# Performance work log

Measured on AMD Instinct MI355X. Metric: run time of the kernel, lower is better.

Reference implementation:

```python
import jax, jax.numpy as jnp
import numpy as np

N = 6144       # nodes
E = 12288      # edges (~2N for a sparse simplicial complex)
NF = 32        # node features
EF = 16        # edge features
NH = [32, 32]  # node_hidden
EH = [16, 16]  # edge_hidden
EPS = 1e-5


def setup_inputs() -> dict:
    key = jax.random.key(0)
    ks = jax.random.split(key, 24)
    s = 0.1  # weight init scale
    inp = {}
    inp["X_n"] = jax.random.normal(ks[0], (N, NF), jnp.float32)
    inp["X_e"] = jax.random.normal(ks[1], (E, EF), jnp.float32)
    # normalized adjacency-like operator (non-negative, row mass ~1)
    inp["A_tilde"] = jax.random.uniform(ks[2], (N, N), jnp.float32) * (1.0 / N)
    # normalized Hodge-1 Laplacian-like operator
    inp["L1_tilde"] = jax.random.normal(ks[3], (E, E), jnp.float32) * (1.0 / np.sqrt(E))
    # incidence-like operator
    inp["B1"] = jax.random.normal(ks[4], (N, E), jnp.float32) * (1.0 / np.sqrt(E))
    # GNN linear layers: weight [out, in] (torch convention)
    inp["gnn_W0"] = jax.random.normal(ks[5], (NH[0], NF), jnp.float32) * s
    inp["gnn_b0"] = jnp.zeros((NH[0],), jnp.float32)
    inp["gnn_W1"] = jax.random.normal(ks[6], (NH[1], NH[0]), jnp.float32) * s
    inp["gnn_b1"] = jnp.zeros((NH[1],), jnp.float32)
    # HoSC layer 0: theta in=EF out=EH[0], BN params
    inp["th_W0"] = jax.random.normal(ks[7], (EH[0], EF), jnp.float32) * s
    inp["th_b0"] = jnp.zeros((EH[0],), jnp.float32)
    inp["bn_g0"] = jnp.ones((EH[0],), jnp.float32)
    inp["bn_b0"] = jnp.zeros((EH[0],), jnp.float32)
    # HoSC layer 1: input collapses to 1 channel (max keepdim)
    inp["th_W1"] = jax.random.normal(ks[8], (EH[1], 1), jnp.float32) * s
    inp["th_b1"] = jnp.zeros((EH[1],), jnp.float32)
    inp["bn_g1"] = jnp.ones((EH[1],), jnp.float32)
    inp["bn_b1"] = jnp.zeros((EH[1],), jnp.float32)
    # head: fc1 in = NH[-1] + len(EH) = 34, out = 2N; fc2 out = 1
    inp["fc1_W"] = jax.random.normal(ks[9], (2 * N, NH[-1] + len(EH)), jnp.float32) * s
    inp["fc1_b"] = jnp.zeros((2 * N,), jnp.float32)
    inp["fc2_W"] = jax.random.normal(ks[10], (1, 2 * N), jnp.float32) * s
    inp["fc2_b"] = jnp.zeros((1,), jnp.float32)
    return inp


def _gnn_layer(A, H, W, b):
    # H <- relu((A @ H) @ W^T + b)
    return jax.nn.relu(jnp.matmul(jnp.matmul(A, H), W.T) + b)


def _hosc_layer(Z, L1, W, b, g, beta):
    Zt = jnp.matmul(Z, W.T) + b            # theta
    Zc = jnp.matmul(L1, Zt)                # Laplacian conv
    m = jnp.mean(Zc, axis=0)               # BatchNorm1d (training-mode batch stats)
    v = jnp.var(Zc, axis=0)
    Zp = jax.nn.relu(g * (Zc - m) * jax.lax.rsqrt(v + EPS) + beta)
    return jnp.max(Zp, axis=1, keepdims=True)  # [E, 1]


def reference(X_n, X_e, A_tilde, L1_tilde, B1,
              gnn_W0, gnn_b0, gnn_W1, gnn_b1,
              th_W0, th_b0, bn_g0, bn_b0,
              th_W1, th_b1, bn_g1, bn_b1,
              fc1_W, fc1_b, fc2_W, fc2_b):
    # GNN over nodes
    H = _gnn_layer(A_tilde, X_n, gnn_W0, gnn_b0)
    H_n = _gnn_layer(A_tilde, H, gnn_W1, gnn_b1)      # [N, NH[-1]]
    # HoSC over edges
    Z0 = _hosc_layer(X_e, L1_tilde, th_W0, th_b0, bn_g0, bn_b0)  # [E, 1]
    Z1 = _hosc_layer(Z0, L1_tilde, th_W1, th_b1, bn_g1, bn_b1)   # [E, 1]
    Z_cat = jnp.concatenate([Z0, Z1], axis=1)         # [E, 2]
    H_e = jnp.matmul(B1, Z_cat)                       # [N, 2]
    # head
    Hcat = jnp.concatenate([H_n, H_e], axis=1)        # [N, 34]
    f = jax.nn.relu(jnp.matmul(Hcat, fc1_W.T) + fc1_b)
    f = jnp.matmul(f, fc2_W.T) + fc2_b                # [N, 1]
    return jax.nn.sigmoid(f).squeeze(-1)              # [N]
```

## Files before the change

kernel.cpp:

```cpp
#include <hip/hip_runtime.h>
#include <hip/hip_cooperative_groups.h>
#include <math.h>

namespace cg = cooperative_groups;

#define NND 6144
#define NED 12288
#define GRID 1024
static constexpr float EPS_BN = 1e-5f;

#define HN_OFF    0
#define HE_OFF    196608
#define ST_OFF    208896
#define Y_OFF     208960
#define T0_OFF    405568
#define ZT_OFF    602176
#define ZC_OFF    798784
#define Z0_OFF    995392
#define Z1_OFF    1007680
#define U_OFF     1019968
#define S_OFF     1032256
#define PP_OFF    1044544

typedef float floatx4 __attribute__((ext_vector_type(4)));

__device__ __forceinline__ float4 ntload4(const float* p) {
  floatx4 v = __builtin_nontemporal_load(reinterpret_cast<const floatx4*>(p));
  return make_float4(v.x, v.y, v.z, v.w);
}
__device__ __forceinline__ float4 ld4(const float* p) {
  return *reinterpret_cast<const float4*>(p);
}
__device__ __forceinline__ void gll16(const float* g, float* l) {
  __builtin_amdgcn_global_load_lds(
      (const __attribute__((address_space(1))) unsigned int*)g,
      (__attribute__((address_space(3))) unsigned int*)l, 16, 0, 0);
}

struct Params {
  const float *X_n, *X_e, *A, *L1, *B1;
  const float *gW0, *gb0, *gW1, *gb1;
  const float *tW0, *tb0, *bng0, *bnb0;
  const float *tW1, *tb1, *bng1, *bnb1;
  const float *fc1W, *fc1b, *fc2W, *fc2b;
  float *ws;
  float *out;
};

template<int PHASE>
__global__ __launch_bounds__(256)
__attribute__((amdgpu_waves_per_eu(4, 4)))
void pipeline(Params p) {
  __shared__ float lds[10240];
  float* sst = &lds[10176];
  float* red = &lds[10208];

  const int tid  = threadIdx.x;
  const int lane = tid & 63;
  const int w    = tid >> 6;
  const int blk  = blockIdx.x;
  const int gtid = blk * 256 + tid;
  constexpr bool ALL = (PHASE == 0);

  float* Hn = p.ws + HN_OFF;
  float* he = p.ws + HE_OFF;
  float* st = p.ws + ST_OFF;
  float* Y  = p.ws + Y_OFF;
  float* T0 = p.ws + T0_OFF;
  float* ZT = p.ws + ZT_OFF;
  float* ZC = p.ws + ZC_OFF;
  float* Z0 = p.ws + Z0_OFF;
  float* Z1 = p.ws + Z1_OFF;
  float* u  = p.ws + U_OFF;
  float* s  = p.ws + S_OFF;
  float* pp = p.ws + PP_OFF;

  auto gemm32 = [&](const float* bias, float* outp) {
    const int rg = w >> 1, cg_ = w & 1;
    const int r0 = blk * 6;
    const int c0 = cg_ * 16;
    float acc[3][16];
    #pragma unroll
    for (int r = 0; r < 3; ++r)
      #pragma unroll
      for (int c = 0; c < 16; ++c) acc[r][c] = 0.f;

    for (int kb = 0; kb < NND; kb += 256) {
      #pragma unroll
      for (int i = 0; i < 8; ++i) {
        const int yr = w * 8 + i;
        gll16(Y + (size_t)yr * NND + kb + lane * 4, &lds[yr * 256]);
      }
      #pragma unroll
      for (int i = 0; i < 2; ++i) {
        const int ar = w * 2 + i;
        if (ar < 6)
          gll16(p.A + (size_t)(r0 + ar) * NND + kb + lane * 4, &lds[8192 + ar * 256]);
      }
      __syncthreads();
      float4 av[3];
      #pragma unroll
      for (int r = 0; r < 3; ++r)
        av[r] = ld4(&lds[8192 + (rg * 3 + r) * 256 + lane * 4]);
      #pragma unroll
      for (int c = 0; c < 16; ++c) {
        const float4 y = ld4(&lds[(c0 + c) * 256 + lane * 4]);
        #pragma unroll
        for (int r = 0; r < 3; ++r) {
          acc[r][c] = fmaf(av[r].x, y.x, acc[r][c]);
          acc[r][c] = fmaf(av[r].y, y.y, acc[r][c]);
          acc[r][c] = fmaf(av[r].z, y.z, acc[r][c]);
          acc[r][c] = fmaf(av[r].w, y.w, acc[r][c]);
        }
      }
      __syncthreads();
    }
    #pragma unroll
    for (int r = 0; r < 3; ++r) {
      float wv[16];
      #pragma unroll
      for (int c = 0; c < 16; ++c) {
        float t = acc[r][c] + __shfl_xor(acc[r][c], 32, 64);
        wv[c] = t + __shfl_xor(t, 16, 64);
      }
      #pragma unroll
      for (int b = 3; b >= 0; --b) {
        const int m = 1 << b;
        const bool hi = (lane & m) != 0;
        #pragma unroll
        for (int i = 0; i < (1 << b); ++i) {
          float x = wv[i], yv = wv[i + (1 << b)];
          float send = hi ? x : yv;
          float recv = __shfl_xor(send, m, 64);
          wv[i] = (hi ? yv : x) + recv;
        }
      }
      if (lane < 16) {
        float v = fmaxf(wv[0] + bias[c0 + lane], 0.f);
        outp[(size_t)(r0 + rg * 3 + r) * 32 + c0 + lane] = v;
      }
    }
  };

  if constexpr (ALL || PHASE == 1) {
    if (blk == 0 && tid < 64) st[tid] = 0.f;
    if (gtid < NND) {
      const int m = gtid;
      float x[32];
      #pragma unroll
      for (int k = 0; k < 32; k += 4) {
        float4 v = ld4(p.X_n + (size_t)m * 32 + k);
        x[k] = v.x; x[k+1] = v.y; x[k+2] = v.z; x[k+3] = v.w;
      }
      #pragma unroll
      for (int oc = 0; oc < 32; ++oc) {
        float acc = 0.f;
        #pragma unroll
        for (int k = 0; k < 32; ++k) acc = fmaf(x[k], p.gW0[oc * 32 + k], acc);
        Y[(size_t)oc * NND + m] = acc;
      }
    } else if (gtid < NND + NED) {
      const int e = gtid - NND;
      float x[16];
      #pragma unroll
      for (int k = 0; k < 16; k += 4) {
        float4 v = ld4(p.X_e + (size_t)e * 16 + k);
        x[k] = v.x; x[k+1] = v.y; x[k+2] = v.z; x[k+3] = v.w;
      }
      #pragma unroll
      for (int oc = 0; oc < 16; ++oc) {
        float acc = p.tb0[oc];
        #pragma unroll
        for (int k = 0; k < 16; ++k) acc = fmaf(x[k], p.tW0[oc * 16 + k], acc);
        ZT[(size_t)oc * NED + e] = acc;
      }
    }
  }
  if constexpr (ALL) cg::this_grid().sync();

  if constexpr (ALL || PHASE == 2) {
    gemm32(p.gb0, T0);

    const int r0 = blk * 12;
    float acc[3][16];
    #pragma unroll
    for (int r = 0; r < 3; ++r)
      #pragma unroll
      for (int c = 0; c < 16; ++c) acc[r][c] = 0.f;

    for (int kb = 0; kb < NED; kb += 256) {
      #pragma unroll
      for (int i = 0; i < 4; ++i) {
        const int yr = w * 4 + i;
        gll16(ZT + (size_t)yr * NED + kb + lane * 4, &lds[yr * 256]);
      }
      #pragma unroll
      for (int i = 0; i < 3; ++i) {
        const int ar = w * 3 + i;
        gll16(p.L1 + (size_t)(r0 + ar) * NED + kb + lane * 4, &lds[4096 + ar * 256]);
      }
      __syncthreads();
      float4 av[3];
      #pragma unroll
      for (int r = 0; r < 3; ++r)
        av[r] = ld4(&lds[4096 + (w * 3 + r) * 256 + lane * 4]);
      #pragma unroll
      for (int c = 0; c < 16; ++c) {
        const float4 y = ld4(&lds[c * 256 + lane * 4]);
        #pragma unroll
        for (int r = 0; r < 3; ++r) {
          acc[r][c] = fmaf(av[r].x, y.x, acc[r][c]);
          acc[r][c] = fmaf(av[r].y, y.y, acc[r][c]);
          acc[r][c] = fmaf(av[r].z, y.z, acc[r][c]);
          acc[r][c] = fmaf(av[r].w, y.w, acc[r][c]);
        }
      }
      __syncthreads();
    }
    float stS = 0.f, stQ = 0.f;
    #pragma unroll
    for (int r = 0; r < 3; ++r) {
      float wv[16];
      #pragma unroll
      for (int c = 0; c < 16; ++c) {
        float t = acc[r][c] + __shfl_xor(acc[r][c], 32, 64);
        wv[c] = t + __shfl_xor(t, 16, 64);
      }
      #pragma unroll
      for (int b = 3; b >= 0; --b) {
        const int m = 1 << b;
        const bool hi = (lane & m) != 0;
        #pragma unroll
        for (int i = 0; i < (1 << b); ++i) {
          float x = wv[i], yv = wv[i + (1 << b)];
          float send = hi ? x : yv;
          float recv = __shfl_xor(send, m, 64);
          wv[i] = (hi ? yv : x) + recv;
        }
      }
      if (lane < 16) {
        const float v = wv[0];
        ZC[(size_t)(r0 + w * 3 + r) * 16 + lane] = v;
        stS += v; stQ += v * v;
      }
    }
    if (tid < 32) sst[tid] = 0.f;
    __syncthreads();
    if (lane < 16) {
      atomicAdd(&sst[lane], stS);
      atomicAdd(&sst[16 + lane], stQ);
    }
    __syncthreads();
    if (tid < 32) atomicAdd(st + tid, sst[tid]);
  }
  if constexpr (ALL) cg::this_grid().sync();

  if constexpr (ALL || PHASE == 3) {
    if (gtid < NND) {
      const int m = gtid;
      float x[32];
      #pragma unroll
      for (int k = 0; k < 32; k += 4) {
        float4 v = ld4(T0 + (size_t)m * 32 + k);
        x[k] = v.x; x[k+1] = v.y; x[k+2] = v.z; x[k+3] = v.w;
      }
      #pragma unroll
      for (int oc = 0; oc < 32; ++oc) {
        float acc = 0.f;
        #pragma unroll
        for (int k = 0; k < 32; ++k) acc = fmaf(x[k], p.gW1[oc * 32 + k], acc);
        Y[(size_t)oc * NND + m] = acc;
      }
    } else if (gtid < NND + NED) {
      const int e = gtid - NND;
      const float invE = 1.f / (float)NED;
      float best = -3.4e38f;
      #pragma unroll
      for (int c = 0; c < 16; ++c) {
        float m = st[c] * invE;
        float var = st[16 + c] * invE - m * m;
        float sc = p.bng0[c] * rsqrtf(var + EPS_BN);
        float sh = p.bnb0[c] - m * sc;
        best = fmaxf(best, fmaf(ZC[(size_t)e * 16 + c], sc, sh));
      }
      Z0[e] = fmaxf(best, 0.f);
    }
  }
  if constexpr (ALL) cg::this_grid().sync();

  if constexpr (ALL || PHASE == 4) {
    gemm32(p.gb1, Hn);

    const int rb = GRID - 1 - blk;
    const int r0 = rb * 12 + w * 3;
    const float* mp[3];
    #pragma unroll
    for (int r = 0; r < 3; ++r) mp[r] = p.L1 + (size_t)(r0 + r) * NED;
    float ua[3] = {0,0,0}, sa[3] = {0,0,0};
    float4 a[3], an[3];
    #pragma unroll
    for (int r = 0; r < 3; ++r) a[r] = ntload4(mp[r] + lane * 4);
    float4 z = ld4(Z0 + lane * 4), zn;
    for (int kb = 0; kb < NED; kb += 256) {
      const int k = kb + lane * 4;
      const bool more = (kb + 256) < NED;
      if (more) {
        #pragma unroll
        for (int r = 0; r < 3; ++r) an[r] = ntload4(mp[r] + k + 256);
        zn = ld4(Z0 + k + 256);
      }
      #pragma unroll
      for (int r = 0; r < 3; ++r) {
        ua[r] += a[r].x*z.x + a[r].y*z.y + a[r].z*z.z + a[r].w*z.w;
        sa[r] += a[r].x + a[r].y + a[r].z + a[r].w;
      }
      if (more) {
        #pragma unroll
        for (int r = 0; r < 3; ++r) a[r] = an[r];
        z = zn;
      }
    }
    #pragma unroll
    for (int r = 0; r < 3; ++r)
      #pragma unroll
      for (int m = 1; m < 64; m <<= 1) {
        ua[r] += __shfl_xor(ua[r], m, 64);
        sa[r] += __shfl_xor(sa[r], m, 64);
      }
    if (lane == 0) {
      float s1 = 0.f, s2 = 0.f, s3 = 0.f, s4 = 0.f, s5 = 0.f;
      #pragma unroll
      for (int r = 0; r < 3; ++r) {
        u[r0 + r] = ua[r]; s[r0 + r] = sa[r];
        s1 += ua[r]; s2 += sa[r];
        s3 += ua[r] * ua[r]; s4 += sa[r] * sa[r]; s5 += ua[r] * sa[r];
      }
      red[w * 5 + 0] = s1; red[w * 5 + 1] = s2; red[w * 5 + 2] = s3;
      red[w * 5 + 3] = s4; red[w * 5 + 4] = s5;
    }
    __syncthreads();
    if (tid < 5)
      atomicAdd(st + 32 + tid, red[tid] + red[5 + tid] + red[10 + tid] + red[15 + tid]);
  }
  if constexpr (ALL) cg::this_grid().sync();

  if constexpr (ALL || PHASE == 5) {
    if (gtid < NED) {
      const int e = gtid;
      const float invE = 1.f / (float)NED;
      const float Su = st[32], Ss = st[33], Suu = st[34], Sss = st[35], Sus = st[36];
      const float uu = u[e], ssv = s[e];
      float best = -3.4e38f;
      #pragma unroll
      for (int c = 0; c < 16; ++c) {
        const float wc = p.tW1[c], bc = p.tb1[c];
        const float mean = (wc * Su + bc * Ss) * invE;
        const float ex2 = (wc * wc * Suu + 2.f * wc * bc * Sus + bc * bc * Sss) * invE;
        const float var = ex2 - mean * mean;
        const float sc = p.bng1[c] * rsqrtf(var + EPS_BN);
        const float sh = p.bnb1[c] - mean * sc;
        best = fmaxf(best, fmaf(wc * uu + bc * ssv, sc, sh));
      }
      Z1[e] = fmaxf(best, 0.f);
    }
  }
  if constexpr (ALL) cg::this_grid().sync();

  if constexpr (ALL || PHASE == 6) {
    const int r0 = blk * 12 + w * 3;
    if (r0 < NND) {
      const float* mp[3];
      #pragma unroll
      for (int r = 0; r < 3; ++r) mp[r] = p.B1 + (size_t)(r0 + r) * NED;
      float uu[3] = {0,0,0}, vv[3] = {0,0,0};
      float4 a[3], an[3];
      #pragma unroll
      for (int r = 0; r < 3; ++r) a[r] = ntload4(mp[r] + lane * 4);
      float4 z = ld4(Z0 + lane * 4), y = ld4(Z1 + lane * 4), zn, yn;
      for (int kb = 0; kb < NED; kb += 256) {
        const int k = kb + lane * 4;
        const bool more = (kb + 256) < NED;
        if (more) {
          #pragma unroll
          for (int r = 0; r < 3; ++r) an[r] = ntload4(mp[r] + k + 256);
          zn = ld4(Z0 + k + 256); yn = ld4(Z1 + k + 256);
        }
        #pragma unroll
        for (int r = 0; r < 3; ++r) {
          uu[r] += a[r].x*z.x + a[r].y*z.y + a[r].z*z.z + a[r].w*z.w;
          vv[r] += a[r].x*y.x + a[r].y*y.y + a[r].z*y.z + a[r].w*y.w;
        }
        if (more) {
          #pragma unroll
          for (int r = 0; r < 3; ++r) a[r] = an[r];
          z = zn; y = yn;
        }
      }
      #pragma unroll
      for (int r = 0; r < 3; ++r)
        #pragma unroll
        for (int m = 1; m < 64; m <<= 1) {
          uu[r] += __shfl_xor(uu[r], m, 64);
          vv[r] += __shfl_xor(vv[r], m, 64);
        }
      if (lane == 0) {
        #pragma unroll
        for (int r = 0; r < 3; ++r) {
          he[(r0 + r) * 2]     = uu[r];
          he[(r0 + r) * 2 + 1] = vv[r];
        }
      }
    }
  }
  if constexpr (ALL) cg::this_grid().sync();

  if constexpr (ALL || PHASE == 7) {
    if (blk < 768) {
      const int nb = blk % 24, jb = blk / 24;
      const int n = nb * 256 + tid;
      float h[34];
      #pragma unroll
      for (int k = 0; k < 32; k += 4) {
        float4 v = ld4(Hn + (size_t)n * 32 + k);
        h[k] = v.x; h[k+1] = v.y; h[k+2] = v.z; h[k+3] = v.w;
      }
      float2 e2 = *reinterpret_cast<const float2*>(he + n * 2);
      h[32] = e2.x; h[33] = e2.y;
      float acc = 0.f;
      const int j0 = jb * 384;
      for (int j = j0; j < j0 + 384; ++j) {
        const float* wp = p.fc1W + (size_t)j * 34;
        float s0 = p.fc1b[j];
        #pragma unroll
        for (int k = 0; k < 34; ++k) s0 = fmaf(h[k], wp[k], s0);
        acc = fmaf(fmaxf(s0, 0.f), p.fc2W[j], acc);
      }
      pp[(size_t)jb * NND + n] = acc;
    }
  }
  if constexpr (ALL) cg::this_grid().sync();

  if constexpr (ALL || PHASE == 8) {
    if (gtid < NND) {
      float acc = 0.f;
      #pragma unroll
      for (int j = 0; j < 32; ++j) acc += pp[(size_t)j * NND + gtid];
      p.out[gtid] = 1.f / (1.f + expf(-(acc + p.fc2b[0])));
    }
  }
}

extern "C" void kernel_launch(void* const* d_in, const int* in_sizes, int n_in,
                              void* d_out, int out_size, void* d_ws, size_t ws_size,
                              hipStream_t stream) {
  Params p;
  p.X_n  = (const float*)d_in[0];
  p.X_e  = (const float*)d_in[1];
  p.A    = (const float*)d_in[2];
  p.L1   = (const float*)d_in[3];
  p.B1   = (const float*)d_in[4];
  p.gW0  = (const float*)d_in[5];
  p.gb0  = (const float*)d_in[6];
  p.gW1  = (const float*)d_in[7];
  p.gb1  = (const float*)d_in[8];
  p.tW0  = (const float*)d_in[9];
  p.tb0  = (const float*)d_in[10];
  p.bng0 = (const float*)d_in[11];
  p.bnb0 = (const float*)d_in[12];
  p.tW1  = (const float*)d_in[13];
  p.tb1  = (const float*)d_in[14];
  p.bng1 = (const float*)d_in[15];
  p.bnb1 = (const float*)d_in[16];
  p.fc1W = (const float*)d_in[17];
  p.fc1b = (const float*)d_in[18];
  p.fc2W = (const float*)d_in[19];
  p.fc2b = (const float*)d_in[20];
  p.ws   = (float*)d_ws;
  p.out  = (float*)d_out;

  int maxBlk = 0;
  hipError_t oe = hipOccupancyMaxActiveBlocksPerMultiprocessor(
      &maxBlk, pipeline<0>, 256, 0);
  bool coop_ok = (oe == hipSuccess) && (maxBlk >= 4);

  if (coop_ok) {
    void* kargs[] = { &p };
    hipError_t le = hipLaunchCooperativeKernel(
        (const void*)&pipeline<0>, dim3(GRID), dim3(256), kargs, 0, stream);
    if (le == hipSuccess) return;
  }

  pipeline<1><<<GRID, 256, 0, stream>>>(p);
  pipeline<2><<<GRID, 256, 0, stream>>>(p);
  pipeline<3><<<GRID, 256, 0, stream>>>(p);
  pipeline<4><<<GRID, 256, 0, stream>>>(p);
  pipeline<5><<<GRID, 256, 0, stream>>>(p);
  pipeline<6><<<GRID, 256, 0, stream>>>(p);
  pipeline<7><<<GRID, 256, 0, stream>>>(p);
  pipeline<8><<<GRID, 256, 0, stream>>>(p);
}
```

Baseline: 711.2 us.

## Split cooperative persistent kernel into separate per-stage kernel launches

Replaces the single cooperative-groups kernel with grid-wide syncs by eleven specialized kernels, each with its own grid size and LDS allocation. Phases that were fused in one launch (A-gemm with L1-gemm, A-gemm with the u/s pass) now run as separate launches. The fc head is reworked to process three nodes per thread, reusing each weight load across them, with a 64-way j split. The aim is to drop grid-sync overhead and the fixed waves_per_eu constraint, at the cost of more launches and the loss of overlap between the node and edge streams.

```diff
diff --git a/kernel.cpp b/kernel.cpp
--- a/kernel.cpp
+++ b/kernel.cpp
@@ -1,12 +1,8 @@
 #include <hip/hip_runtime.h>
-#include <hip/hip_cooperative_groups.h>
 #include <math.h>
-
-namespace cg = cooperative_groups;
 
 #define NND 6144
 #define NED 12288
-#define GRID 1024
 static constexpr float EPS_BN = 1e-5f;
 
 #define HN_OFF    0
@@ -37,465 +33,462 @@
       (__attribute__((address_space(3))) unsigned int*)l, 16, 0, 0);
 }
 
-struct Params {
-  const float *X_n, *X_e, *A, *L1, *B1;
-  const float *gW0, *gb0, *gW1, *gb1;
-  const float *tW0, *tb0, *bng0, *bnb0;
-  const float *tW1, *tb1, *bng1, *bnb1;
-  const float *fc1W, *fc1b, *fc2W, *fc2b;
-  float *ws;
-  float *out;
-};
-
-template<int PHASE>
 __global__ __launch_bounds__(256)
-__attribute__((amdgpu_waves_per_eu(4, 4)))
-void pipeline(Params p) {
-  __shared__ float lds[10240];
-  float* sst = &lds[10176];
-  float* red = &lds[10208];
-
-  const int tid  = threadIdx.x;
-  const int lane = tid & 63;
-  const int w    = tid >> 6;
-  const int blk  = blockIdx.x;
-  const int gtid = blk * 256 + tid;
-  constexpr bool ALL = (PHASE == 0);
-
-  float* Hn = p.ws + HN_OFF;
-  float* he = p.ws + HE_OFF;
-  float* st = p.ws + ST_OFF;
-  float* Y  = p.ws + Y_OFF;
-  float* T0 = p.ws + T0_OFF;
-  float* ZT = p.ws + ZT_OFF;
-  float* ZC = p.ws + ZC_OFF;
-  float* Z0 = p.ws + Z0_OFF;
-  float* Z1 = p.ws + Z1_OFF;
-  float* u  = p.ws + U_OFF;
-  float* s  = p.ws + S_OFF;
-  float* pp = p.ws + PP_OFF;
-
-  auto gemm32 = [&](const float* bias, float* outp) {
-    const int rg = w >> 1, cg_ = w & 1;
-    const int r0 = blk * 6;
-    const int c0 = cg_ * 16;
-    float acc[3][16];
+void k1_prep(const float* __restrict__ X_n, const float* __restrict__ X_e,
+             const float* __restrict__ gW0, const float* __restrict__ tW0,
+             const float* __restrict__ tb0, float* __restrict__ Y,
+             float* __restrict__ ZT, float* __restrict__ st) {
+  const int gtid = blockIdx.x * 256 + threadIdx.x;
+  if (blockIdx.x == 0 && threadIdx.x < 64) st[threadIdx.x] = 0.f;
+  if (gtid < NND) {
+    const int m = gtid;
+    float x[32];
+    #pragma unroll
+    for (int k = 0; k < 32; k += 4) {
+      float4 v = ld4(X_n + (size_t)m * 32 + k);
+      x[k] = v.x; x[k+1] = v.y; x[k+2] = v.z; x[k+3] = v.w;
+    }
+    #pragma unroll
+    for (int oc = 0; oc < 32; ++oc) {
+      float acc = 0.f;
+      #pragma unroll
+      for (int k = 0; k < 32; ++k) acc = fmaf(x[k], gW0[oc * 32 + k], acc);
+      Y[(size_t)oc * NND + m] = acc;
+    }
+  } else if (gtid < NND + NED) {
+    const int e = gtid - NND;
+    float x[16];
+    #pragma unroll
+    for (int k = 0; k < 16; k += 4) {
+      float4 v = ld4(X_e + (size_t)e * 16 + k);
+      x[k] = v.x; x[k+1] = v.y; x[k+2] = v.z; x[k+3] = v.w;
+    }
+    #pragma unroll
+    for (int oc = 0; oc < 16; ++oc) {
+      float acc = tb0[oc];
+      #pragma unroll
+      for (int k = 0; k < 16; ++k) acc = fmaf(x[k], tW0[oc * 16 + k], acc);
+      ZT[(size_t)oc * NED + e] = acc;
+    }
+  }
+}
+
+__global__ __launch_bounds__(256, 4)
+void k2_gemm32(const float* __restrict__ A, const float* __restrict__ Y,
+               const float* __restrict__ bias, float* __restrict__ outp) {
+  __shared__ float lds[9728];
+  const int tid = threadIdx.x, lane = tid & 63, w = tid >> 6;
+  const int rg = w >> 1, cg_ = w & 1;
+  const int r0 = blockIdx.x * 6;
+  const int c0 = cg_ * 16;
+  float acc[3][16];
+  #pragma unroll
+  for (int r = 0; r < 3; ++r)
+    #pragma unroll
+    for (int c = 0; c < 16; ++c) acc[r][c] = 0.f;
+
+  for (int kb = 0; kb < NND; kb += 256) {
+    #pragma unroll
+    for (int i = 0; i < 8; ++i) {
+      const int yr = w * 8 + i;
+      gll16(Y + (size_t)yr * NND + kb + lane * 4, &lds[yr * 256]);
+    }
+    #pragma unroll
+    for (int i = 0; i < 2; ++i) {
+      const int ar = w * 2 + i;
+      if (ar < 6)
+        gll16(A + (size_t)(r0 + ar) * NND + kb + lane * 4, &lds[8192 + ar * 256]);
+    }
+    __syncthreads();
+    float4 av[3];
     #pragma unroll
     for (int r = 0; r < 3; ++r)
-      #pragma unroll
-      for (int c = 0; c < 16; ++c) acc[r][c] = 0.f;
-
-    for (int kb = 0; kb < NND; kb += 256) {
-      #pragma unroll
-      for (int i = 0; i < 8; ++i) {
-        const int yr = w * 8 + i;
-        gll16(Y + (size_t)yr * NND + kb + lane * 4, &lds[yr * 256]);
+      av[r] = ld4(&lds[8192 + (rg * 3 + r) * 256 + lane * 4]);
+    #pragma unroll
+    for (int c = 0; c < 16; ++c) {
+      const float4 y = ld4(&lds[(c0 + c) * 256 + lane * 4]);
+      #pragma unroll
+      for (int r = 0; r < 3; ++r) {
+        acc[r][c] = fmaf(av[r].x, y.x, acc[r][c]);
+        acc[r][c] = fmaf(av[r].y, y.y, acc[r][c]);
+        acc[r][c] = fmaf(av[r].z, y.z, acc[r][c]);
+        acc[r][c] = fmaf(av[r].w, y.w, acc[r][c]);
       }
-      #pragma unroll
-      for (int i = 0; i < 2; ++i) {
-        const int ar = w * 2 + i;
-        if (ar < 6)
-          gll16(p.A + (size_t)(r0 + ar) * NND + kb + lane * 4, &lds[8192 + ar * 256]);
+    }
+    __syncthreads();
+  }
+  #pragma unroll
+  for (int r = 0; r < 3; ++r) {
+    float wv[16];
+    #pragma unroll
+    for (int c = 0; c < 16; ++c) {
+      float t = acc[r][c] + __shfl_xor(acc[r][c], 32, 64);
+      wv[c] = t + __shfl_xor(t, 16, 64);
+    }
+    #pragma unroll
+    for (int b = 3; b >= 0; --b) {
+      const int m = 1 << b;
+      const bool hi = (lane & m) != 0;
+      #pragma unroll
+      for (int i = 0; i < (1 << b); ++i) {
+        float x = wv[i], yv = wv[i + (1 << b)];
+        float send = hi ? x : yv;
+        float recv = __shfl_xor(send, m, 64);
+        wv[i] = (hi ? yv : x) + recv;
       }
-      __syncthreads();
-      float4 av[3];
-      #pragma unroll
-      for (int r = 0; r < 3; ++r)
-        av[r] = ld4(&lds[8192 + (rg * 3 + r) * 256 + lane * 4]);
-      #pragma unroll
-      for (int c = 0; c < 16; ++c) {
-        const float4 y = ld4(&lds[(c0 + c) * 256 + lane * 4]);
-        #pragma unroll
-        for (int r = 0; r < 3; ++r) {
-          acc[r][c] = fmaf(av[r].x, y.x, acc[r][c]);
-          acc[r][c] = fmaf(av[r].y, y.y, acc[r][c]);
-          acc[r][c] = fmaf(av[r].z, y.z, acc[r][c]);
-          acc[r][c] = fmaf(av[r].w, y.w, acc[r][c]);
-        }
+    }
+    if (lane < 16) {
+      float v = fmaxf(wv[0] + bias[c0 + lane], 0.f);
+      outp[(size_t)(r0 + rg * 3 + r) * 32 + c0 + lane] = v;
+    }
+  }
+}
+
+__global__ __launch_bounds__(256)
+void k3_small(const float* __restrict__ T0, const float* __restrict__ gW1,
+              float* __restrict__ Y) {
+  const int m = blockIdx.x * 256 + threadIdx.x;
+  float x[32];
+  #pragma unroll
+  for (int k = 0; k < 32; k += 4) {
+    float4 v = ld4(T0 + (size_t)m * 32 + k);
+    x[k] = v.x; x[k+1] = v.y; x[k+2] = v.z; x[k+3] = v.w;
+  }
+  #pragma unroll
+  for (int oc = 0; oc < 32; ++oc) {
+    float acc = 0.f;
+    #pragma unroll
+    for (int k = 0; k < 32; ++k) acc = fmaf(x[k], gW1[oc * 32 + k], acc);
+    Y[(size_t)oc * NND + m] = acc;
+  }
+}
+
+__global__ __launch_bounds__(256, 4)
+void k5_l1gemm(const float* __restrict__ L1, const float* __restrict__ ZT,
+               float* __restrict__ ZC, float* __restrict__ st) {
+  __shared__ float lds[7168];
+  __shared__ float sst[32];
+  const int tid = threadIdx.x, lane = tid & 63, w = tid >> 6;
+  const int r0 = blockIdx.x * 12;
+  float acc[3][16];
+  #pragma unroll
+  for (int r = 0; r < 3; ++r)
+    #pragma unroll
+    for (int c = 0; c < 16; ++c) acc[r][c] = 0.f;
+
+  for (int kb = 0; kb < NED; kb += 256) {
+    #pragma unroll
+    for (int i = 0; i < 4; ++i) {
+      const int yr = w * 4 + i;
+      gll16(ZT + (size_t)yr * NED + kb + lane * 4, &lds[yr * 256]);
+    }
+    #pragma unroll
+    for (int i = 0; i < 3; ++i) {
+      const int ar = w * 3 + i;
+      gll16(L1 + (size_t)(r0 + ar) * NED + kb + lane * 4, &lds[4096 + ar * 256]);
+    }
+    __syncthreads();
+    float4 av[3];
+    #pragma unroll
+    for (int r = 0; r < 3; ++r)
+      av[r] = ld4(&lds[4096 + (w * 3 + r) * 256 + lane * 4]);
+    #pragma unroll
+    for (int c = 0; c < 16; ++c) {
+      const float4 y = ld4(&lds[c * 256 + lane * 4]);
+      #pragma unroll
+      for (int r = 0; r < 3; ++r) {
+        acc[r][c] = fmaf(av[r].x, y.x, acc[r][c]);
+        acc[r][c] = fmaf(av[r].y, y.y, acc[r][c]);
+        acc[r][c] = fmaf(av[r].z, y.z, acc[r][c]);
+        acc[r][c] = fmaf(av[r].w, y.w, acc[r][c]);
       }
-      __syncthreads();
+    }
+    __syncthreads();
+  }
+  float stS = 0.f, stQ = 0.f;
+  #pragma unroll
+  for (int r = 0; r < 3; ++r) {
+    float wv[16];
+    #pragma unroll
+    for (int c = 0; c < 16; ++c) {
+      float t = acc[r][c] + __shfl_xor(acc[r][c], 32, 64);
+      wv[c] = t + __shfl_xor(t, 16, 64);
+    }
+    #pragma unroll
+    for (int b = 3; b >= 0; --b) {
+      const int m = 1 << b;
+      const bool hi = (lane & m) != 0;
+      #pragma unroll
+      for (int i = 0; i < (1 << b); ++i) {
+        float x = wv[i], yv = wv[i + (1 << b)];
+        float send = hi ? x : yv;
+        float recv = __shfl_xor(send, m, 64);
+        wv[i] = (hi ? yv : x) + recv;
+      }
+    }
+    if (lane < 16) {
+      const float v = wv[0];
+      ZC[(size_t)(r0 + w * 3 + r) * 16 + lane] = v;
+      stS += v; stQ += v * v;
+    }
+  }
+  if (tid < 32) sst[tid] = 0.f;
+  __syncthreads();
+  if (lane < 16) {
+    atomicAdd(&sst[lane], stS);
+    atomicAdd(&sst[16 + lane], stQ);
+  }
+  __syncthreads();
+  if (tid < 32) atomicAdd(st + tid, sst[tid]);
+}
+
+__global__ __launch_bounds__(256)
+void k6_bnmax(const float* __restrict__ ZC, const float* __restrict__ st,
+              const float* __restrict__ g, const float* __restrict__ beta,
+              float* __restrict__ Z0) {
+  const int e = blockIdx.x * 256 + threadIdx.x;
+  const float invE = 1.f / (float)NED;
+  float best = -3.4e38f;
+  #pragma unroll
+  for (int c = 0; c < 16; ++c) {
+    float m = st[c] * invE;
+    float var = st[16 + c] * invE - m * m;
+    float sc = g[c] * rsqrtf(var + EPS_BN);
+    float sh = beta[c] - m * sc;
+    best = fmaxf(best, fmaf(ZC[(size_t)e * 16 + c], sc, sh));
+  }
+  Z0[e] = fmaxf(best, 0.f);
+}
+
+__global__ __launch_bounds__(256, 4)
+void k7_uspass(const float* __restrict__ L1, const float* __restrict__ Z0,
+               float* __restrict__ u, float* __restrict__ s,
+               float* __restrict__ st5) {
+  __shared__ float red[20];
+  const int tid = threadIdx.x, lane = tid & 63, w = tid >> 6;
+  const int rb = gridDim.x - 1 - blockIdx.x;
+  const int r0 = rb * 12 + w * 3;
+  const float* mp[3];
+  #pragma unroll
+  for (int r = 0; r < 3; ++r) mp[r] = L1 + (size_t)(r0 + r) * NED;
+  float ua[3] = {0,0,0}, sa[3] = {0,0,0};
+  float4 a[3], an[3];
+  #pragma unroll
+  for (int r = 0; r < 3; ++r) a[r] = ntload4(mp[r] + lane * 4);
+  float4 z = ld4(Z0 + lane * 4), zn;
+  for (int kb = 0; kb < NED; kb += 256) {
+    const int k = kb + lane * 4;
+    const bool more = (kb + 256) < NED;
+    if (more) {
+      #pragma unroll
+      for (int r = 0; r < 3; ++r) an[r] = ntload4(mp[r] + k + 256);
+      zn = ld4(Z0 + k + 256);
     }
     #pragma unroll
     for (int r = 0; r < 3; ++r) {
-      float wv[16];
-      #pragma unroll
-      for (int c = 0; c < 16; ++c) {
-        float t = acc[r][c] + __shfl_xor(acc[r][c], 32, 64);
-        wv[c] = t + __shfl_xor(t, 16, 64);
-      }
-      #pragma unroll
-      for (int b = 3; b >= 0; --b) {
-        const int m = 1 << b;
-        const bool hi = (lane & m) != 0;
-        #pragma unroll
-        for (int i = 0; i < (1 << b); ++i) {
-          float x = wv[i], yv = wv[i + (1 << b)];
-          float send = hi ? x : yv;
-          float recv = __shfl_xor(send, m, 64);
-          wv[i] = (hi ? yv : x) + recv;
-        }
-      }
-      if (lane < 16) {
-        float v = fmaxf(wv[0] + bias[c0 + lane], 0.f);
-        outp[(size_t)(r0 + rg * 3 + r) * 32 + c0 + lane] = v;
-      }
-    }
-  };
-
-  if constexpr (ALL || PHASE == 1) {
-    if (blk == 0 && tid < 64) st[tid] = 0.f;
-    if (gtid < NND) {
-      const int m = gtid;
-      float x[32];
-      #pragma unroll
-      for (int k = 0; k < 32; k += 4) {
-        float4 v = ld4(p.X_n + (size_t)m * 32 + k);
-        x[k] = v.x; x[k+1] = v.y; x[k+2] = v.z; x[k+3] = v.w;
-      }
-      #pragma unroll
-      for (int oc = 0; oc < 32; ++oc) {
-        float acc = 0.f;
-        #pragma unroll
-        for (int k = 0; k < 32; ++k) acc = fmaf(x[k], p.gW0[oc * 32 + k], acc);
-        Y[(size_t)oc * NND + m] = acc;
-      }
-    } else if (gtid < NND + NED) {
-      const int e = gtid - NND;
-      float x[16];
-      #pragma unroll
-      for (int k = 0; k < 16; k += 4) {
-        float4 v = ld4(p.X_e + (size_t)e * 16 + k);
-        x[k] = v.x; x[k+1] = v.y; x[k+2] = v.z; x[k+3] = v.w;
-      }
-      #pragma unroll
-      for (int oc = 0; oc < 16; ++oc) {
-        float acc = p.tb0[oc];
-        #pragma unroll
-        for (int k = 0; k < 16; ++k) acc = fmaf(x[k], p.tW0[oc * 16 + k], acc);
-        ZT[(size_t)oc * NED + e] = acc;
-      }
-    }
-  }
-  if constexpr (ALL) cg::this_grid().sync();
-
-  if constexpr (ALL || PHASE == 2) {
-    gemm32(p.gb0, T0);
-
-    const int r0 = blk * 12;
-    float acc[3][16];
-    #pragma unroll
-    for (int r = 0; r < 3; ++r)
-      #pragma unroll
-      for (int c = 0; c < 16; ++c) acc[r][c] = 0.f;
-
-    for (int kb = 0; kb < NED; kb += 256) {
-      #pragma unroll
-      for (int i = 0; i < 4; ++i) {
-        const int yr = w * 4 + i;
-        gll16(ZT + (size_t)yr * NED + kb + lane * 4, &lds[yr * 256]);
-      }
-      #pragma unroll
-      for (int i = 0; i < 3; ++i) {
-        const int ar = w * 3 + i;
-        gll16(p.L1 + (size_t)(r0 + ar) * NED + kb + lane * 4, &lds[4096 + ar * 256]);
-      }
-      __syncthreads();
-      float4 av[3];
-      #pragma unroll
-      for (int r = 0; r < 3; ++r)
-        av[r] = ld4(&lds[4096 + (w * 3 + r) * 256 + lane * 4]);
-      #pragma unroll
-      for (int c = 0; c < 16; ++c) {
-        const float4 y = ld4(&lds[c * 256 + lane * 4]);
-        #pragma unroll
-        for (int r = 0; r < 3; ++r) {
-          acc[r][c] = fmaf(av[r].x, y.x, acc[r][c]);
-          acc[r][c] = fmaf(av[r].y, y.y, acc[r][c]);
-          acc[r][c] = fmaf(av[r].z, y.z, acc[r][c]);
-          acc[r][c] = fmaf(av[r].w, y.w, acc[r][c]);
-        }
-      }
-      __syncthreads();
-    }
-    float stS = 0.f, stQ = 0.f;
+      ua[r] += a[r].x*z.x + a[r].y*z.y + a[r].z*z.z + a[r].w*z.w;
+      sa[r] += a[r].x + a[r].y + a[r].z + a[r].w;
+    }
+    if (more) {
+      #pragma unroll
+      for (int r = 0; r < 3; ++r) a[r] = an[r];
+      z = zn;
+    }
+  }
+  #pragma unroll
+  for (int r = 0; r < 3; ++r)
+    #pragma unroll
+    for (int m = 1; m < 64; m <<= 1) {
+      ua[r] += __shfl_xor(ua[r], m, 64);
+      sa[r] += __shfl_xor(sa[r], m, 64);
+    }
+  if (lane == 0) {
+    float s1 = 0.f, s2 = 0.f, s3 = 0.f, s4 = 0.f, s5 = 0.f;
     #pragma unroll
     for (int r = 0; r < 3; ++r) {
-      float wv[16];
-      #pragma unroll
-      for (int c = 0; c < 16; ++c) {
-        float t = acc[r][c] + __shfl_xor(acc[r][c], 32, 64);
-        wv[c] = t + __shfl_xor(t, 16, 64);
-      }
-      #pragma unroll
-      for (int b = 3; b >= 0; --b) {
-        const int m = 1 << b;
-        const bool hi = (lane & m) != 0;
-        #pragma unroll
-        for (int i = 0; i < (1 << b); ++i) {
-          float x = wv[i], yv = wv[i + (1 << b)];
-          float send = hi ? x : yv;
-          float recv = __shfl_xor(send, m, 64);
-          wv[i] = (hi ? yv : x) + recv;
-        }
-      }
-      if (lane < 16) {
-        const float v = wv[0];
-        ZC[(size_t)(r0 + w * 3 + r) * 16 + lane] = v;
-        stS += v; stQ += v * v;
-      }
-    }
-    if (tid < 32) sst[tid] = 0.f;
-    __syncthreads();
-    if (lane < 16) {
-      atomicAdd(&sst[lane], stS);
-      atomicAdd(&sst[16 + lane], stQ);
-    }
-    __syncthreads();
-    if (tid < 32) atomicAdd(st + tid, sst[tid]);
-  }
-  if constexpr (ALL) cg::this_grid().sync();
-
-  if constexpr (ALL || PHASE == 3) {
-    if (gtid < NND) {
-      const int m = gtid;
-      float x[32];
-      #pragma unroll
-      for (int k = 0; k < 32; k += 4) {
-        float4 v = ld4(T0 + (size_t)m * 32 + k);
-        x[k] = v.x; x[k+1] = v.y; x[k+2] = v.z; x[k+3] = v.w;
-      }
-      #pragma unroll
-      for (int oc = 0; oc < 32; ++oc) {
-        float acc = 0.f;
-        #pragma unroll
-        for (int k = 0; k < 32; ++k) acc = fmaf(x[k], p.gW1[oc * 32 + k], acc);
-        Y[(size_t)oc * NND + m] = acc;
-      }
-    } else if (gtid < NND + NED) {
-      const int e = gtid - NND;
-      const float invE = 1.f / (float)NED;
-      float best = -3.4e38f;
-      #pragma unroll
-      for (int c = 0; c < 16; ++c) {
-        float m = st[c] * invE;
-        float var = st[16 + c] * invE - m * m;
-        float sc = p.bng0[c] * rsqrtf(var + EPS_BN);
-        float sh = p.bnb0[c] - m * sc;
-        best = fmaxf(best, fmaf(ZC[(size_t)e * 16 + c], sc, sh));
-      }
-      Z0[e] = fmaxf(best, 0.f);
-    }
-  }
-  if constexpr (ALL) cg::this_grid().sync();
-
-  if constexpr (ALL || PHASE == 4) {
-    gemm32(p.gb1, Hn);
-
-    const int rb = GRID - 1 - blk;
-    const int r0 = rb * 12 + w * 3;
-    const float* mp[3];
-    #pragma unroll
-    for (int r = 0; r < 3; ++r) mp[r] = p.L1 + (size_t)(r0 + r) * NED;
-    float ua[3] = {0,0,0}, sa[3] = {0,0,0};
-    float4 a[3], an[3];
-    #pragma unroll
-    for (int r = 0; r < 3; ++r) a[r] = ntload4(mp[r] + lane * 4);
-    float4 z = ld4(Z0 + lane * 4), zn;
-    for (int kb = 0; kb < NED; kb += 256) {
-      const int k = kb + lane * 4;
-      const bool more = (kb + 256) < NED;
-      if (more) {
-        #pragma unroll
-        for (int r = 0; r < 3; ++r) an[r] = ntload4(mp[r] + k + 256);
-        zn = ld4(Z0 + k + 256);
-      }
-      #pragma unroll
-      for (int r = 0; r < 3; ++r) {
-        ua[r] += a[r].x*z.x + a[r].y*z.y + a[r].z*z.z + a[r].w*z.w;
-        sa[r] += a[r].x + a[r].y + a[r].z + a[r].w;
-      }
-      if (more) {
-        #pragma unroll
-        for (int r = 0; r < 3; ++r) a[r] = an[r];
-        z = zn;
-      }
-    }
-    #pragma unroll
-    for (int r = 0; r < 3; ++r)
-      #pragma unroll
-      for (int m = 1; m < 64; m <<= 1) {
-        ua[r] += __shfl_xor(ua[r], m, 64);
-        sa[r] += __shfl_xor(sa[r], m, 64);
-      }
-    if (lane == 0) {
-      float s1 = 0.f, s2 = 0.f, s3 = 0.f, s4 = 0.f, s5 = 0.f;
-      #pragma unroll
-      for (int r = 0; r < 3; ++r) {
-        u[r0 + r] = ua[r]; s[r0 + r] = sa[r];
-        s1 += ua[r]; s2 += sa[r];
-        s3 += ua[r] * ua[r]; s4 += sa[r] * sa[r]; s5 += ua[r] * sa[r];
-      }
-      red[w * 5 + 0] = s1; red[w * 5 + 1] = s2; red[w * 5 + 2] = s3;
-      red[w * 5 + 3] = s4; red[w * 5 + 4] = s5;
-    }
-    __syncthreads();
-    if (tid < 5)
-      atomicAdd(st + 32 + tid, red[tid] + red[5 + tid] + red[10 + tid] + red[15 + tid]);
-  }
-  if constexpr (ALL) cg::this_grid().sync();
-
-  if constexpr (ALL || PHASE == 5) {
-    if (gtid < NED) {
-      const int e = gtid;
-      const float invE = 1.f / (float)NED;
-      const float Su = st[32], Ss = st[33], Suu = st[34], Sss = st[35], Sus = st[36];
-      const float uu = u[e], ssv = s[e];
-      float best = -3.4e38f;
-      #pragma unroll
-      for (int c = 0; c < 16; ++c) {
-        const float wc = p.tW1[c], bc = p.tb1[c];
-        const float mean = (wc * Su + bc * Ss) * invE;
-        const float ex2 = (wc * wc * Suu + 2.f * wc * bc * Sus + bc * bc * Sss) * invE;
-        const float var = ex2 - mean * mean;
-        const float sc = p.bng1[c] * rsqrtf(var + EPS_BN);
-        const float sh = p.bnb1[c] - mean * sc;
-        best = fmaxf(best, fmaf(wc * uu + bc * ssv, sc, sh));
-      }
-      Z1[e] = fmaxf(best, 0.f);
-    }
-  }
-  if constexpr (ALL) cg::this_grid().sync();
-
-  if constexpr (ALL || PHASE == 6) {
-    const int r0 = blk * 12 + w * 3;
-    if (r0 < NND) {
-      const float* mp[3];
-      #pragma unroll
-      for (int r = 0; r < 3; ++r) mp[r] = p.B1 + (size_t)(r0 + r) * NED;
-      float uu[3] = {0,0,0}, vv[3] = {0,0,0};
-      float4 a[3], an[3];
-      #pragma unroll
-      for (int r = 0; r < 3; ++r) a[r] = ntload4(mp[r] + lane * 4);
-      float4 z = ld4(Z0 + lane * 4), y = ld4(Z1 + lane * 4), zn, yn;
-      for (int kb = 0; kb < NED; kb += 256) {
-        const int k = kb + lane * 4;
-        const bool more = (kb + 256) < NED;
-        if (more) {
-          #pragma unroll
-          for (int r = 0; r < 3; ++r) an[r] = ntload4(mp[r] + k + 256);
-          zn = ld4(Z0 + k + 256); yn = ld4(Z1 + k + 256);
-        }
-        #pragma unroll
-        for (int r = 0; r < 3; ++r) {
-          uu[r] += a[r].x*z.x + a[r].y*z.y + a[r].z*z.z + a[r].w*z.w;
-          vv[r] += a[r].x*y.x + a[r].y*y.y + a[r].z*y.z + a[r].w*y.w;
-        }
-        if (more) {
-          #pragma unroll
-          for (int r = 0; r < 3; ++r) a[r] = an[r];
-          z = zn; y = yn;
-        }
-      }
-      #pragma unroll
-      for (int r = 0; r < 3; ++r)
-        #pragma unroll
-        for (int m = 1; m < 64; m <<= 1) {
-          uu[r] += __shfl_xor(uu[r], m, 64);
-          vv[r] += __shfl_xor(vv[r], m, 64);
-        }
-      if (lane == 0) {
-        #pragma unroll
-        for (int r = 0; r < 3; ++r) {
-          he[(r0 + r) * 2]     = uu[r];
-          he[(r0 + r) * 2 + 1] = vv[r];
-        }
-      }
-    }
-  }
-  if constexpr (ALL) cg::this_grid().sync();
-
-  if constexpr (ALL || PHASE == 7) {
-    if (blk < 768) {
-      const int nb = blk % 24, jb = blk / 24;
-      const int n = nb * 256 + tid;
-      float h[34];
-      #pragma unroll
-      for (int k = 0; k < 32; k += 4) {
-        float4 v = ld4(Hn + (size_t)n * 32 + k);
-        h[k] = v.x; h[k+1] = v.y; h[k+2] = v.z; h[k+3] = v.w;
-      }
-      float2 e2 = *reinterpret_cast<const float2*>(he + n * 2);
-      h[32] = e2.x; h[33] = e2.y;
-      float acc = 0.f;
-      const int j0 = jb * 384;
-      for (int j = j0; j < j0 + 384; ++j) {
-        const float* wp = p.fc1W + (size_t)j * 34;
-        float s0 = p.fc1b[j];
-        #pragma unroll
-        for (int k = 0; k < 34; ++k) s0 = fmaf(h[k], wp[k], s0);
-        acc = fmaf(fmaxf(s0, 0.f), p.fc2W[j], acc);
-      }
-      pp[(size_t)jb * NND + n] = acc;
-    }
-  }
-  if constexpr (ALL) cg::this_grid().sync();
-
-  if constexpr (ALL || PHASE == 8) {
-    if (gtid < NND) {
-      float acc = 0.f;
-      #pragma unroll
-      for (int j = 0; j < 32; ++j) acc += pp[(size_t)j * NND + gtid];
-      p.out[gtid] = 1.f / (1.f + expf(-(acc + p.fc2b[0])));
-    }
-  }
+      u[r0 + r] = ua[r]; s[r0 + r] = sa[r];
+      s1 += ua[r]; s2 += sa[r];
+      s3 += ua[r] * ua[r]; s4 += sa[r] * sa[r]; s5 += ua[r] * sa[r];
+    }
+    red[w * 5 + 0] = s1; red[w * 5 + 1] = s2; red[w * 5 + 2] = s3;
+    red[w * 5 + 3] = s4; red[w * 5 + 4] = s5;
+  }
+  __syncthreads();
+  if (tid < 5)
+    atomicAdd(st5 + tid, red[tid] + red[5 + tid] + red[10 + tid] + red[15 + tid]);
+}
+
+__global__ __launch_bounds__(256)
+void k8_z1(const float* __restrict__ u, const float* __restrict__ s,
+           const float* __restrict__ st5, const float* __restrict__ W1,
+           const float* __restrict__ b1, const float* __restrict__ g,
+           const float* __restrict__ beta, float* __restrict__ Z1) {
+  const int e = blockIdx.x * 256 + threadIdx.x;
+  const float invE = 1.f / (float)NED;
+  const float Su = st5[0], Ss = st5[1], Suu = st5[2], Sss = st5[3], Sus = st5[4];
+  const float uu = u[e], ssv = s[e];
+  float best = -3.4e38f;
+  #pragma unroll
+  for (int c = 0; c < 16; ++c) {
+    const float wc = W1[c], bc = b1[c];
+    const float mean = (wc * Su + bc * Ss) * invE;
+    const float ex2 = (wc * wc * Suu + 2.f * wc * bc * Sus + bc * bc * Sss) * invE;
+    const float var = ex2 - mean * mean;
+    const float sc = g[c] * rsqrtf(var + EPS_BN);
+    const float sh = beta[c] - mean * sc;
+    best = fmaxf(best, fmaf(wc * uu + bc * ssv, sc, sh));
+  }
+  Z1[e] = fmaxf(best, 0.f);
+}
+
+__global__ __launch_bounds__(256, 4)
+void k9_b1pass(const float* __restrict__ B1, const float* __restrict__ Z0,
+               const float* __restrict__ Z1, float* __restrict__ he) {
+  const int lane = threadIdx.x & 63, w = threadIdx.x >> 6;
+  const int r0 = blockIdx.x * 12 + w * 3;
+  const float* mp[3];
+  #pragma unroll
+  for (int r = 0; r < 3; ++r) mp[r] = B1 + (size_t)(r0 + r) * NED;
+  float uu[3] = {0,0,0}, vv[3] = {0,0,0};
+  float4 a[3], an[3];
+  #pragma unroll
+  for (int r = 0; r < 3; ++r) a[r] = ntload4(mp[r] + lane * 4);
+  float4 z = ld4(Z0 + lane * 4), y = ld4(Z1 + lane * 4), zn, yn;
+  for (int kb = 0; kb < NED; kb += 256) {
+    const int k = kb + lane * 4;
+    const bool more = (kb + 256) < NED;
+    if (more) {
+      #pragma unroll
+      for (int r = 0; r < 3; ++r) an[r] = ntload4(mp[r] + k + 256);
+      zn = ld4(Z0 + k + 256); yn = ld4(Z1 + k + 256);
+    }
+    #pragma unroll
+    for (int r = 0; r < 3; ++r) {
+      uu[r] += a[r].x*z.x + a[r].y*z.y + a[r].z*z.z + a[r].w*z.w;
+      vv[r] += a[r].x*y.x + a[r].y*y.y + a[r].z*y.z + a[r].w*y.w;
+    }
+    if (more) {
+      #pragma unroll
+      for (int r = 0; r < 3; ++r) a[r] = an[r];
+      z = zn; y = yn;
+    }
+  }
+  #pragma unroll
+  for (int r = 0; r < 3; ++r)
+    #pragma unroll
+    for (int m = 1; m < 64; m <<= 1) {
+      uu[r] += __shfl_xor(uu[r], m, 64);
+      vv[r] += __shfl_xor(vv[r], m, 64);
+    }
+  if (lane == 0) {
+    #pragma unroll
+    for (int r = 0; r < 3; ++r) {
+      he[(r0 + r) * 2]     = uu[r];
+      he[(r0 + r) * 2 + 1] = vv[r];
+    }
+  }
+}
+
+__global__ __launch_bounds__(256, 2)
+void k10_head(const float* __restrict__ Hn, const float* __restrict__ he,
+              const float* __restrict__ W1, const float* __restrict__ b1,
+              const float* __restrict__ w2, float* __restrict__ pp) {
+  const int t = threadIdx.x;
+  const int nb = blockIdx.x;
+  const int jb = blockIdx.y;
+  int n[3];
+  float h[3][34];
+  float acc[3] = {0.f, 0.f, 0.f};
+  #pragma unroll
+  for (int i = 0; i < 3; ++i) {
+    n[i] = nb * 768 + i * 256 + t;
+    #pragma unroll
+    for (int k = 0; k < 32; k += 4) {
+      float4 v = ld4(Hn + (size_t)n[i] * 32 + k);
+      h[i][k] = v.x; h[i][k+1] = v.y; h[i][k+2] = v.z; h[i][k+3] = v.w;
+    }
+    float2 e2 = *reinterpret_cast<const float2*>(he + n[i] * 2);
+    h[i][32] = e2.x; h[i][33] = e2.y;
+  }
+  const int j0 = jb * 192;
+  for (int j = j0; j < j0 + 192; ++j) {
+    const float* wp = W1 + (size_t)j * 34;
+    const float bj = b1[j], vj = w2[j];
+    float s0 = bj, s1 = bj, s2 = bj;
+    #pragma unroll
+    for (int k = 0; k < 34; ++k) {
+      const float wk = wp[k];
+      s0 = fmaf(h[0][k], wk, s0);
+      s1 = fmaf(h[1][k], wk, s1);
+      s2 = fmaf(h[2][k], wk, s2);
+    }
+    acc[0] += fmaxf(s0, 0.f) * vj;
+    acc[1] += fmaxf(s1, 0.f) * vj;
+    acc[2] += fmaxf(s2, 0.f) * vj;
+  }
+  #pragma unroll
+  for (int i = 0; i < 3; ++i) pp[(size_t)jb * NND + n[i]] = acc[i];
+}
+
+__global__ __launch_bounds__(256)
+void k11_final(const float* __restrict__ pp, const float* __restrict__ b2,
+               float* __restrict__ out) {
+  const int i = blockIdx.x * 256 + threadIdx.x;
+  float acc = 0.f;
+  #pragma unroll
+  for (int j = 0; j < 64; ++j) acc += pp[(size_t)j * NND + i];
+  out[i] = 1.f / (1.f + expf(-(acc + b2[0])));
 }
 
 extern "C" void kernel_launch(void* const* d_in, const int* in_sizes, int n_in,
                               void* d_out, int out_size, void* d_ws, size_t ws_size,
                               hipStream_t stream) {
-  Params p;
-  p.X_n  = (const float*)d_in[0];
-  p.X_e  = (const float*)d_in[1];
-  p.A    = (const float*)d_in[2];
-  p.L1   = (const float*)d_in[3];
-  p.B1   = (const float*)d_in[4];
-  p.gW0  = (const float*)d_in[5];
-  p.gb0  = (const float*)d_in[6];
-  p.gW1  = (const float*)d_in[7];
-  p.gb1  = (const float*)d_in[8];
-  p.tW0  = (const float*)d_in[9];
-  p.tb0  = (const float*)d_in[10];
-  p.bng0 = (const float*)d_in[11];
-  p.bnb0 = (const float*)d_in[12];
-  p.tW1  = (const float*)d_in[13];
-  p.tb1  = (const float*)d_in[14];
-  p.bng1 = (const float*)d_in[15];
-  p.bnb1 = (const float*)d_in[16];
-  p.fc1W = (const float*)d_in[17];
-  p.fc1b = (const float*)d_in[18];
-  p.fc2W = (const float*)d_in[19];
-  p.fc2b = (const float*)d_in[20];
-  p.ws   = (float*)d_ws;
-  p.out  = (float*)d_out;
-
-  int maxBlk = 0;
-  hipError_t oe = hipOccupancyMaxActiveBlocksPerMultiprocessor(
-      &maxBlk, pipeline<0>, 256, 0);
-  bool coop_ok = (oe == hipSuccess) && (maxBlk >= 4);
-
-  if (coop_ok) {
-    void* kargs[] = { &p };
-    hipError_t le = hipLaunchCooperativeKernel(
-        (const void*)&pipeline<0>, dim3(GRID), dim3(256), kargs, 0, stream);
-    if (le == hipSuccess) return;
-  }
-
-  pipeline<1><<<GRID, 256, 0, stream>>>(p);
-  pipeline<2><<<GRID, 256, 0, stream>>>(p);
-  pipeline<3><<<GRID, 256, 0, stream>>>(p);
-  pipeline<4><<<GRID, 256, 0, stream>>>(p);
-  pipeline<5><<<GRID, 256, 0, stream>>>(p);
-  pipeline<6><<<GRID, 256, 0, stream>>>(p);
-  pipeline<7><<<GRID, 256, 0, stream>>>(p);
-  pipeline<8><<<GRID, 256, 0, stream>>>(p);
-}
+  const float* X_n  = (const float*)d_in[0];
+  const float* X_e  = (const float*)d_in[1];
+  const float* A    = (const float*)d_in[2];
+  const float* L1   = (const float*)d_in[3];
+  const float* B1   = (const float*)d_in[4];
+  const float* gW0  = (const float*)d_in[5];
+  const float* gb0  = (const float*)d_in[6];
+  const float* gW1  = (const float*)d_in[7];
+  const float* gb1  = (const float*)d_in[8];
+  const float* tW0  = (const float*)d_in[9];
+  const float* tb0  = (const float*)d_in[10];
+  const float* bng0 = (const float*)d_in[11];
+  const float* bnb0 = (const float*)d_in[12];
+  const float* tW1  = (const float*)d_in[13];
+  const float* tb1  = (const float*)d_in[14];
+  const float* bng1 = (const float*)d_in[15];
+  const float* bnb1 = (const float*)d_in[16];
+  const float* fc1W = (const float*)d_in[17];
+  const float* fc1b = (const float*)d_in[18];
+  const float* fc2W = (const float*)d_in[19];
+  const float* fc2b = (const float*)d_in[20];
+
+  float* ws = (float*)d_ws;
+  float* Hn = ws + HN_OFF;
+  float* he = ws + HE_OFF;
+  float* st = ws + ST_OFF;
+  float* Y  = ws + Y_OFF;
+  float* T0 = ws + T0_OFF;
+  float* ZT = ws + ZT_OFF;
+  float* ZC = ws + ZC_OFF;
+  float* Z0 = ws + Z0_OFF;
+  float* Z1 = ws + Z1_OFF;
+  float* u  = ws + U_OFF;
+  float* s  = ws + S_OFF;
+  float* pp = ws + PP_OFF;
+  float* out = (float*)d_out;
+
+  k1_prep<<<72, 256, 0, stream>>>(X_n, X_e, gW0, tW0, tb0, Y, ZT, st);
+  k2_gemm32<<<1024, 256, 0, stream>>>(A, Y, gb0, T0);
+  k3_small<<<24, 256, 0, stream>>>(T0, gW1, Y);
+  k2_gemm32<<<1024, 256, 0, stream>>>(A, Y, gb1, Hn);
+  k5_l1gemm<<<1024, 256, 0, stream>>>(L1, ZT, ZC, st);
+  k6_bnmax<<<48, 256, 0, stream>>>(ZC, st, bng0, bnb0, Z0);
+  k7_uspass<<<1024, 256, 0, stream>>>(L1, Z0, u, s, st + 32);
+  k8_z1<<<48, 256, 0, stream>>>(u, s, st + 32, tW1, tb1, bng1, bnb1, Z1);
+  k9_b1pass<<<512, 256, 0, stream>>>(B1, Z0, Z1, he);
+  k10_head<<<dim3(8, 64), 256, 0, stream>>>(Hn, he, fc1W, fc1b, fc2W, pp);
+  k11_final<<<24, 256, 0, stream>>>(pp, fc2b, out);
+}
```

New measurement: 647.3 us. -9.0%, faster.
